# Performance work log

Hardware: AMD Instinct MI355X
Metric: run time of the kernel (lower is better)

## Reference

```python
import jax, jax.numpy as jnp
import numpy as np

N, E, DIN, DOUT, H = 50000, 800000, 256, 128, 8
DH = DOUT // H  # per-head dim = 16


def setup_inputs() -> dict:
    key = jax.random.key(0)
    k1, k2, k3, k4, k5 = jax.random.split(key, 5)
    x = jax.random.normal(k1, (N, DIN), dtype=jnp.float32)
    edge_index = jax.random.randint(k2, (2, E), 0, N)
    W_trans = jax.random.normal(k3, (DOUT, DIN), dtype=jnp.float32) / np.sqrt(DIN).astype(np.float32)
    W_att = jax.random.normal(k4, (1, 2 * DH), dtype=jnp.float32) / np.sqrt(2 * DH).astype(np.float32)
    b_att = jax.random.normal(k5, (1,), dtype=jnp.float32) * 0.01
    return {"x": x, "W_trans": W_trans, "W_att": W_att, "b_att": b_att, "edge_index": edge_index}


def reference(x, W_trans, W_att, b_att, edge_index):
    n = x.shape[0]
    # append self-loops (as in the torch module)
    loops = jnp.arange(n, dtype=edge_index.dtype)
    ei = jnp.concatenate([edge_index, jnp.stack([loops, loops])], axis=1)  # [2, E+N]
    src, dst = ei[0], ei[1]

    # linear transform, split heads: [n, H, DH]
    h = (x @ W_trans.T).reshape(n, H, DH)
    h_i = h[src]  # [Etot, H, DH]
    h_j = h[dst]  # [Etot, H, DH]

    # per-edge attention score: concat -> linear -> leaky_relu(0.2)
    s = jnp.concatenate([h_i, h_j], axis=-1) @ W_att.T + b_att  # [Etot, H, 1]
    s = jnp.where(s >= 0, s, 0.2 * s)

    # softmax(dim=0)*exp_sum/scatter_add(exp) == exp(s)/segment_sum(exp(s)) per dst node
    e = jnp.exp(s)
    denom = jax.ops.segment_sum(e, dst, num_segments=n)  # [n, H, 1]
    att = e / denom[dst]

    out = jax.ops.segment_sum(h_i * att, dst, num_segments=n)  # [n, H, DH]
    return out.reshape(n, DOUT)  # head_fusion='cat'
```

## Files before the change

### kernel.cpp

```cpp
#include <hip/hip_runtime.h>


constexpr int DIN  = 256;
constexpr int DOUT = 128;
constexpr int H    = 8;
constexpr int CAP  = 5120;
constexpr int CHUNK = 4096;

typedef __attribute__((ext_vector_type(8))) short bf16x8;
typedef __attribute__((ext_vector_type(4))) float f32x4;

__device__ __forceinline__ float lrelu(float s) { return s >= 0.0f ? s : 0.2f * s; }

__device__ __forceinline__ unsigned short f2bf(float f) {
  unsigned u = __float_as_uint(f);
  u += 0x7FFF + ((u >> 16) & 1);
  return (unsigned short)(u >> 16);
}
__device__ __forceinline__ float bflo(unsigned u) { return __uint_as_float(u << 16); }
__device__ __forceinline__ float bfhi(unsigned u) { return __uint_as_float(u & 0xFFFF0000u); }

__device__ __forceinline__ int wave_incl_scan(int v, int lane) {
#pragma unroll
  for (int d = 1; d < 64; d <<= 1) {
    int t = __shfl_up(v, d, 64);
    if (lane >= d) v += t;
  }
  return v;
}

__global__ void conv_w(const float* __restrict__ W, unsigned short* __restrict__ Wbf,
                       int n, int* __restrict__ bcount, int nb) {
  int i = blockIdx.x * blockDim.x + threadIdx.x;
  if (i < n) Wbf[i] = f2bf(W[i]);
  if (blockIdx.x == 0 && threadIdx.x < nb) bcount[threadIdx.x] = 0;
}

__global__ __launch_bounds__(256, 2) void bp_gemm(const float* __restrict__ x,
                                                  const unsigned short* __restrict__ Wbf,
                                                  unsigned short* __restrict__ hbf, int N,
                                                  const int* __restrict__ ei,
                                                  int* __restrict__ bcount,
                                                  unsigned* __restrict__ pair_buf,
                                                  int E, int nb, int bp_blocks) {
  __shared__ __align__(16) unsigned short Wlds[DOUT * DIN];
  if ((int)blockIdx.x < bp_blocks) {
    int* hist  = (int*)Wlds;
    int* gbase = hist + 256;
    int c0 = blockIdx.x * CHUNK;
    hist[threadIdx.x] = 0;
    __syncthreads();
    int dcache[16];
#pragma unroll
    for (int q = 0; q < 16; ++q) {
      int e = c0 + q * 256 + threadIdx.x;
      dcache[q] = (e < E) ? ei[E + e] : -1;
      if (dcache[q] >= 0) atomicAdd(&hist[dcache[q] >> 8], 1);
    }
    __syncthreads();
    if (threadIdx.x < nb) {
      int c = hist[threadIdx.x];
      gbase[threadIdx.x] = c ? atomicAdd(&bcount[threadIdx.x], c) : 0;
    }
    __syncthreads();
    hist[threadIdx.x] = 0;
    __syncthreads();
#pragma unroll
    for (int q = 0; q < 16; ++q) {
      int e = c0 + q * 256 + threadIdx.x;
      if (dcache[q] >= 0) {
        int s = ei[e];
        int bk = dcache[q] >> 8;
        int r = atomicAdd(&hist[bk], 1);
        pair_buf[bk * CAP + gbase[bk] + r] = ((unsigned)s << 8) | (unsigned)(dcache[q] & 255);
      }
    }
    return;
  }
  {
    const int tid = threadIdx.x;
#pragma unroll
    for (int i = 0; i < 16; ++i) {
      int c = i * 256 + tid;
      int t = c >> 9, ks = (c >> 6) & 7, L = c & 63;
      const unsigned short* gp = Wbf + ((t * 16 + (L & 15)) * DIN + ks * 32 + (L >> 4) * 8);
      *(bf16x8*)&Wlds[c * 8] = *(const bf16x8*)gp;
    }
  }
  __syncthreads();
  int wid = ((int)blockIdx.x - bp_blocks) * 4 + (threadIdx.x >> 6);
  int m0 = wid * 32;
  if (m0 >= N) return;
  int lane = threadIdx.x & 63;
  int mr = lane & 15, kg = lane >> 4;
  int r0 = m0 + mr;       if (r0 >= N) r0 = N - 1;
  int r1 = m0 + 16 + mr;  if (r1 >= N) r1 = N - 1;
  const float* xr0 = x + (size_t)r0 * DIN + kg * 8;
  const float* xr1 = x + (size_t)r1 * DIN + kg * 8;
  const unsigned short* fb = Wlds + lane * 8;

  f32x4 acc[2][8];
#pragma unroll
  for (int mt = 0; mt < 2; ++mt)
#pragma unroll
    for (int t = 0; t < 8; ++t) acc[mt][t] = (f32x4){0.f, 0.f, 0.f, 0.f};

  float4 p00 = *(const float4*)xr0, p01 = *(const float4*)(xr0 + 4);
  float4 p10 = *(const float4*)xr1, p11 = *(const float4*)(xr1 + 4);
#pragma unroll
  for (int ks = 0; ks < 8; ++ks) {
    bf16x8 a0, a1;
    a0[0] = (short)f2bf(p00.x); a0[1] = (short)f2bf(p00.y);
    a0[2] = (short)f2bf(p00.z); a0[3] = (short)f2bf(p00.w);
    a0[4] = (short)f2bf(p01.x); a0[5] = (short)f2bf(p01.y);
    a0[6] = (short)f2bf(p01.z); a0[7] = (short)f2bf(p01.w);
    a1[0] = (short)f2bf(p10.x); a1[1] = (short)f2bf(p10.y);
    a1[2] = (short)f2bf(p10.z); a1[3] = (short)f2bf(p10.w);
    a1[4] = (short)f2bf(p11.x); a1[5] = (short)f2bf(p11.y);
    a1[6] = (short)f2bf(p11.z); a1[7] = (short)f2bf(p11.w);
    if (ks < 7) {
      p00 = *(const float4*)(xr0 + (ks + 1) * 32);
      p01 = *(const float4*)(xr0 + (ks + 1) * 32 + 4);
      p10 = *(const float4*)(xr1 + (ks + 1) * 32);
      p11 = *(const float4*)(xr1 + (ks + 1) * 32 + 4);
    }
#pragma unroll
    for (int t = 0; t < 8; ++t) {
      bf16x8 b = *(const bf16x8*)(fb + ((t * 8 + ks) << 9));
      acc[0][t] = __builtin_amdgcn_mfma_f32_16x16x32_bf16(a0, b, acc[0][t], 0, 0, 0);
      acc[1][t] = __builtin_amdgcn_mfma_f32_16x16x32_bf16(a1, b, acc[1][t], 0, 0, 0);
    }
  }
#pragma unroll
  for (int mt = 0; mt < 2; ++mt)
#pragma unroll
    for (int t = 0; t < 8; ++t)
#pragma unroll
      for (int r = 0; r < 4; ++r) {
        int row = m0 + mt * 16 + kg * 4 + r;
        if (row < N) hbf[(size_t)row * DOUT + t * 16 + mr] = f2bf(acc[mt][t][r]);
      }
}

__global__ __launch_bounds__(256) void fs_ns(const unsigned* __restrict__ pair_buf,
                                             const int* __restrict__ bcount,
                                             int* __restrict__ offsets,
                                             unsigned short* __restrict__ src_sorted,
                                             const unsigned short* __restrict__ hbf,
                                             const float* __restrict__ Wa,
                                             float* __restrict__ a_src,
                                             float* __restrict__ a_dst,
                                             int N, int E, int nb) {
  __shared__ int cnt[256];
  __shared__ int cur[256];
  __shared__ int redS[256];
  __shared__ int wsumS[4];
  const int t = threadIdx.x;
  if ((int)blockIdx.x >= nb) {
    int idx = ((int)blockIdx.x - nb) * 256 + t;
    if (idx >= N * H) return;
    int v = idx >> 3, hh = idx & 7;
    const unsigned short* hp = hbf + (size_t)v * DOUT + hh * 16;
    uint4 p0 = *(const uint4*)hp;
    uint4 p1 = *(const uint4*)(hp + 8);
    float hv[16];
    hv[0] = bflo(p0.x); hv[1] = bfhi(p0.x); hv[2] = bflo(p0.y); hv[3] = bfhi(p0.y);
    hv[4] = bflo(p0.z); hv[5] = bfhi(p0.z); hv[6] = bflo(p0.w); hv[7] = bfhi(p0.w);
    hv[8] = bflo(p1.x); hv[9] = bfhi(p1.x); hv[10] = bflo(p1.y); hv[11] = bfhi(p1.y);
    hv[12] = bflo(p1.z); hv[13] = bfhi(p1.z); hv[14] = bflo(p1.w); hv[15] = bfhi(p1.w);
    float s1 = 0.f, s2 = 0.f;
#pragma unroll
    for (int d = 0; d < 16; ++d) {
      s1 += hv[d] * Wa[d];
      s2 += hv[d] * Wa[16 + d];
    }
    a_src[idx] = s1;
    a_dst[idx] = s2;
    return;
  }
  const int B = blockIdx.x;
  const int node0 = B * 256;
  const int v = node0 + t;
  const int valid = (v < N);
  cnt[t] = valid ? 1 : 0;
  __syncthreads();
  const int cntE = bcount[B];
  const unsigned* reg = pair_buf + B * CAP;
  for (int i = t; i < cntE; i += 256)
    atomicAdd(&cnt[reg[i] & 255], 1);
  redS[t] = (t < B) ? bcount[t] : 0;
  __syncthreads();
  for (int s = 128; s > 0; s >>= 1) {
    if (t < s) redS[t] += redS[t + s];
    __syncthreads();
  }
  const int csr_base = redS[0] + node0;
  int val = cnt[t];
  int lane = t & 63, wv = t >> 6;
  int inc = wave_incl_scan(val, lane);
  if (lane == 63) wsumS[wv] = inc;
  __syncthreads();
  int base = 0;
  for (int q = 0; q < wv; ++q) base += wsumS[q];
  int ex = base + inc - val;
  cur[t] = ex + 1;
  if (valid) {
    offsets[v] = csr_base + ex;
    src_sorted[csr_base + ex] = (unsigned short)v;
  }
  if (B == 0 && t == 0) offsets[N] = E + N;
  __syncthreads();
  for (int i = t; i < cntE; i += 256) {
    unsigned p = reg[i];
    int k = atomicAdd(&cur[p & 255], 1);
    src_sorted[csr_base + k] = (unsigned short)(p >> 8);
  }
}

__global__ __launch_bounds__(256) void aggregate(const unsigned short* __restrict__ hbf,
                                                 const float* __restrict__ a_src,
                                                 const float* __restrict__ a_dst,
                                                 const float* __restrict__ b_att,
                                                 const int* __restrict__ offsets,
                                                 const unsigned short* __restrict__ src_sorted,
                                                 float* __restrict__ out, int N) {
  int wid = blockIdx.x * 4 + (threadIdx.x >> 6);
  if (wid >= N) return;
  int lane = threadIdx.x & 63;
  int g = lane >> 4, sl = lane & 15;
  int head = sl >> 1;
  float adv = a_dst[wid * H + head] + b_att[0];
  int beg = offsets[wid], end = offsets[wid + 1];
  float a0 = 0, a1 = 0, a2 = 0, a3 = 0, a4 = 0, a5 = 0, a6 = 0, a7 = 0, den = 0;
  for (int j0 = beg; j0 < end; j0 += 8) {
    int ja = j0 + g, jb = j0 + 4 + g;
    bool va = ja < end, vb = jb < end;
    int sa = src_sorted[va ? ja : beg];
    int sb = src_sorted[vb ? jb : beg];
    float asa = a_src[sa * H + head];
    float asb = a_src[sb * H + head];
    uint4 ua = *(const uint4*)(hbf + sa * DOUT + sl * 8);
    uint4 ub = *(const uint4*)(hbf + sb * DOUT + sl * 8);
    float ea = va ? __expf(lrelu(asa + adv)) : 0.f;
    float eb = vb ? __expf(lrelu(asb + adv)) : 0.f;
    den += ea + eb;
    a0 += ea * bflo(ua.x) + eb * bflo(ub.x);
    a1 += ea * bfhi(ua.x) + eb * bfhi(ub.x);
    a2 += ea * bflo(ua.y) + eb * bflo(ub.y);
    a3 += ea * bfhi(ua.y) + eb * bfhi(ub.y);
    a4 += ea * bflo(ua.z) + eb * bflo(ub.z);
    a5 += ea * bfhi(ua.z) + eb * bfhi(ub.z);
    a6 += ea * bflo(ua.w) + eb * bflo(ub.w);
    a7 += ea * bfhi(ua.w) + eb * bfhi(ub.w);
  }
  den += __shfl_xor(den, 16, 64); den += __shfl_xor(den, 32, 64);
  a0 += __shfl_xor(a0, 16, 64); a0 += __shfl_xor(a0, 32, 64);
  a1 += __shfl_xor(a1, 16, 64); a1 += __shfl_xor(a1, 32, 64);
  a2 += __shfl_xor(a2, 16, 64); a2 += __shfl_xor(a2, 32, 64);
  a3 += __shfl_xor(a3, 16, 64); a3 += __shfl_xor(a3, 32, 64);
  a4 += __shfl_xor(a4, 16, 64); a4 += __shfl_xor(a4, 32, 64);
  a5 += __shfl_xor(a5, 16, 64); a5 += __shfl_xor(a5, 32, 64);
  a6 += __shfl_xor(a6, 16, 64); a6 += __shfl_xor(a6, 32, 64);
  a7 += __shfl_xor(a7, 16, 64); a7 += __shfl_xor(a7, 32, 64);
  float inv = 1.0f / den;
  if (g == 0) {
    float4 o = make_float4(a0 * inv, a1 * inv, a2 * inv, a3 * inv);
    *(float4*)&out[wid * DOUT + sl * 8] = o;
  } else if (g == 1) {
    float4 o = make_float4(a4 * inv, a5 * inv, a6 * inv, a7 * inv);
    *(float4*)&out[wid * DOUT + sl * 8 + 4] = o;
  }
}

extern "C" void kernel_launch(void* const* d_in, const int* in_sizes, int n_in,
                              void* d_out, int out_size, void* d_ws, size_t ws_size,
                              hipStream_t stream) {
  const float* x     = (const float*)d_in[0];
  const float* W     = (const float*)d_in[1];
  const float* Wa    = (const float*)d_in[2];
  const float* b_att = (const float*)d_in[3];
  const int*   ei    = (const int*)d_in[4];
  const int N  = in_sizes[0] / DIN;
  const int E  = in_sizes[4] / 2;
  const int NB = (N + 255) / 256;
  float* out = (float*)d_out;

  char* p = (char*)d_ws;
  auto take = [&p](size_t bytes) {
    uintptr_t u = ((uintptr_t)p + 15) & ~(uintptr_t)15;
    p = (char*)(u + bytes);
    return (void*)u;
  };
  unsigned short* hbf = (unsigned short*)take((size_t)N * DOUT * 2);
  unsigned short* Wbf = (unsigned short*)take((size_t)DOUT * DIN * 2);
  float* a_src        = (float*)take((size_t)N * H * 4);
  float* a_dst        = (float*)take((size_t)N * H * 4);
  int* bcount         = (int*)take((size_t)NB * 4);
  unsigned* pair_buf  = (unsigned*)take((size_t)NB * CAP * 4);
  int* offsets        = (int*)take((size_t)(N + 1) * 4);
  unsigned short* src_sorted = (unsigned short*)take((size_t)(E + N + 16) * 2);

  dim3 b256(256);
  const int bp_blocks   = (E + CHUNK - 1) / CHUNK;
  const int gemm_blocks = ((N + 31) / 32 + 3) / 4;
  const int ns_blocks   = (N * H + 255) / 256;

  conv_w<<<dim3((DOUT * DIN + 255) / 256), b256, 0, stream>>>(W, Wbf, DOUT * DIN, bcount, NB);
  bp_gemm<<<dim3(bp_blocks + gemm_blocks), b256, 0, stream>>>(
      x, Wbf, hbf, N, ei, bcount, pair_buf, E, NB, bp_blocks);
  fs_ns<<<dim3(NB + ns_blocks), b256, 0, stream>>>(
      pair_buf, bcount, offsets, src_sorted, hbf, Wa, a_src, a_dst, N, E, NB);
  aggregate<<<dim3((N + 3) / 4), b256, 0, stream>>>(hbf, a_src, a_dst, b_att, offsets,
                                                    src_sorted, out, N);
}
```

Baseline: 172.0 us.

## Replace bucketed pair-buffer CSR build with global degree count plus atomic scatter

The two-level bucket sort of edges (per-256-node buckets in a fixed-capacity pair buffer, then a local sort per bucket) is replaced by a direct per-node degree count with global atomics, a prefix sum inside fs_ns, and a separate scatter kernel that places each source into CSR slots with global atomicAdd on a per-node cursor. This removes the fixed bucket capacity and the LDS histogram passes, but adds a kernel launch, heavier global atomic traffic, and a per-block serial prefix over all earlier degrees (O(N) reads per block). Neighbour order within a node becomes nondeterministic.

```diff
diff --git a/kernel.cpp b/kernel.cpp
--- a/kernel.cpp
+++ b/kernel.cpp
@@ -4,7 +4,6 @@
 constexpr int DIN  = 256;
 constexpr int DOUT = 128;
 constexpr int H    = 8;
-constexpr int CAP  = 5120;
 constexpr int CHUNK = 4096;
 
 typedef __attribute__((ext_vector_type(8))) short bf16x8;
@@ -30,50 +29,25 @@
 }
 
 __global__ void conv_w(const float* __restrict__ W, unsigned short* __restrict__ Wbf,
-                       int n, int* __restrict__ bcount, int nb) {
+                       int n, int* __restrict__ deg, int N) {
   int i = blockIdx.x * blockDim.x + threadIdx.x;
   if (i < n) Wbf[i] = f2bf(W[i]);
-  if (blockIdx.x == 0 && threadIdx.x < nb) bcount[threadIdx.x] = 0;
-}
-
-__global__ __launch_bounds__(256, 2) void bp_gemm(const float* __restrict__ x,
-                                                  const unsigned short* __restrict__ Wbf,
-                                                  unsigned short* __restrict__ hbf, int N,
-                                                  const int* __restrict__ ei,
-                                                  int* __restrict__ bcount,
-                                                  unsigned* __restrict__ pair_buf,
-                                                  int E, int nb, int bp_blocks) {
+  if (i < N) deg[i] = 0;
+}
+
+__global__ __launch_bounds__(256, 2) void cnt_gemm(const float* __restrict__ x,
+                                                   const unsigned short* __restrict__ Wbf,
+                                                   unsigned short* __restrict__ hbf, int N,
+                                                   const int* __restrict__ ei,
+                                                   int* __restrict__ deg,
+                                                   int E, int bp_blocks) {
   __shared__ __align__(16) unsigned short Wlds[DOUT * DIN];
   if ((int)blockIdx.x < bp_blocks) {
-    int* hist  = (int*)Wlds;
-    int* gbase = hist + 256;
     int c0 = blockIdx.x * CHUNK;
-    hist[threadIdx.x] = 0;
-    __syncthreads();
-    int dcache[16];
 #pragma unroll
     for (int q = 0; q < 16; ++q) {
       int e = c0 + q * 256 + threadIdx.x;
-      dcache[q] = (e < E) ? ei[E + e] : -1;
-      if (dcache[q] >= 0) atomicAdd(&hist[dcache[q] >> 8], 1);
-    }
-    __syncthreads();
-    if (threadIdx.x < nb) {
-      int c = hist[threadIdx.x];
-      gbase[threadIdx.x] = c ? atomicAdd(&bcount[threadIdx.x], c) : 0;
-    }
-    __syncthreads();
-    hist[threadIdx.x] = 0;
-    __syncthreads();
-#pragma unroll
-    for (int q = 0; q < 16; ++q) {
-      int e = c0 + q * 256 + threadIdx.x;
-      if (dcache[q] >= 0) {
-        int s = ei[e];
-        int bk = dcache[q] >> 8;
-        int r = atomicAdd(&hist[bk], 1);
-        pair_buf[bk * CAP + gbase[bk] + r] = ((unsigned)s << 8) | (unsigned)(dcache[q] & 255);
-      }
+      if (e < E) atomicAdd(&deg[ei[E + e]], 1);
     }
     return;
   }
@@ -142,17 +116,15 @@
       }
 }
 
-__global__ __launch_bounds__(256) void fs_ns(const unsigned* __restrict__ pair_buf,
-                                             const int* __restrict__ bcount,
+__global__ __launch_bounds__(256) void fs_ns(const int* __restrict__ deg,
                                              int* __restrict__ offsets,
+                                             int* __restrict__ cur,
                                              unsigned short* __restrict__ src_sorted,
                                              const unsigned short* __restrict__ hbf,
                                              const float* __restrict__ Wa,
                                              float* __restrict__ a_src,
                                              float* __restrict__ a_dst,
                                              int N, int E, int nb) {
-  __shared__ int cnt[256];
-  __shared__ int cur[256];
   __shared__ int redS[256];
   __shared__ int wsumS[4];
   const int t = threadIdx.x;
@@ -182,20 +154,16 @@
   const int node0 = B * 256;
   const int v = node0 + t;
   const int valid = (v < N);
-  cnt[t] = valid ? 1 : 0;
-  __syncthreads();
-  const int cntE = bcount[B];
-  const unsigned* reg = pair_buf + B * CAP;
-  for (int i = t; i < cntE; i += 256)
-    atomicAdd(&cnt[reg[i] & 255], 1);
-  redS[t] = (t < B) ? bcount[t] : 0;
+  int part = 0;
+  for (int j = t; j < node0; j += 256) part += deg[j];
+  redS[t] = part;
   __syncthreads();
   for (int s = 128; s > 0; s >>= 1) {
     if (t < s) redS[t] += redS[t + s];
     __syncthreads();
   }
   const int csr_base = redS[0] + node0;
-  int val = cnt[t];
+  int val = valid ? deg[v] + 1 : 0;
   int lane = t & 63, wv = t >> 6;
   int inc = wave_incl_scan(val, lane);
   if (lane == 63) wsumS[wv] = inc;
@@ -203,17 +171,25 @@
   int base = 0;
   for (int q = 0; q < wv; ++q) base += wsumS[q];
   int ex = base + inc - val;
-  cur[t] = ex + 1;
   if (valid) {
     offsets[v] = csr_base + ex;
     src_sorted[csr_base + ex] = (unsigned short)v;
+    cur[v] = csr_base + ex + 1;
   }
   if (B == 0 && t == 0) offsets[N] = E + N;
-  __syncthreads();
-  for (int i = t; i < cntE; i += 256) {
-    unsigned p = reg[i];
-    int k = atomicAdd(&cur[p & 255], 1);
-    src_sorted[csr_base + k] = (unsigned short)(p >> 8);
+}
+
+__global__ __launch_bounds__(256) void scatter(const int* __restrict__ ei,
+                                               int* __restrict__ cur,
+                                               unsigned short* __restrict__ src_sorted,
+                                               int E) {
+  int i0 = blockIdx.x * blockDim.x + threadIdx.x;
+  int stride = gridDim.x * blockDim.x;
+  for (int e = i0; e < E; e += stride) {
+    int s = ei[e];
+    int d = ei[E + e];
+    int k = atomicAdd(&cur[d], 1);
+    src_sorted[k] = (unsigned short)s;
   }
 }
 
@@ -295,21 +271,23 @@
   unsigned short* Wbf = (unsigned short*)take((size_t)DOUT * DIN * 2);
   float* a_src        = (float*)take((size_t)N * H * 4);
   float* a_dst        = (float*)take((size_t)N * H * 4);
-  int* bcount         = (int*)take((size_t)NB * 4);
-  unsigned* pair_buf  = (unsigned*)take((size_t)NB * CAP * 4);
+  int* deg            = (int*)take((size_t)N * 4);
+  int* cur            = (int*)take((size_t)N * 4);
   int* offsets        = (int*)take((size_t)(N + 1) * 4);
   unsigned short* src_sorted = (unsigned short*)take((size_t)(E + N + 16) * 2);
 
   dim3 b256(256);
+  const int cw_blocks   = (N > DOUT * DIN ? N + 255 : DOUT * DIN + 255) / 256;
   const int bp_blocks   = (E + CHUNK - 1) / CHUNK;
   const int gemm_blocks = ((N + 31) / 32 + 3) / 4;
   const int ns_blocks   = (N * H + 255) / 256;
 
-  conv_w<<<dim3((DOUT * DIN + 255) / 256), b256, 0, stream>>>(W, Wbf, DOUT * DIN, bcount, NB);
-  bp_gemm<<<dim3(bp_blocks + gemm_blocks), b256, 0, stream>>>(
-      x, Wbf, hbf, N, ei, bcount, pair_buf, E, NB, bp_blocks);
+  conv_w<<<dim3(cw_blocks), b256, 0, stream>>>(W, Wbf, DOUT * DIN, deg, N);
+  cnt_gemm<<<dim3(bp_blocks + gemm_blocks), b256, 0, stream>>>(
+      x, Wbf, hbf, N, ei, deg, E, bp_blocks);
   fs_ns<<<dim3(NB + ns_blocks), b256, 0, stream>>>(
-      pair_buf, bcount, offsets, src_sorted, hbf, Wa, a_src, a_dst, N, E, NB);
+      deg, offsets, cur, src_sorted, hbf, Wa, a_src, a_dst, N, E, NB);
+  scatter<<<dim3(1024), b256, 0, stream>>>(ei, cur, src_sorted, E);
   aggregate<<<dim3((N + 3) / 4), b256, 0, stream>>>(hbf, a_src, a_dst, b_att, offsets,
                                                     src_sorted, out, N);
 }
```

Measured after the change: 243.0 us. 1.41x slower.
